# Kernel optimization log

Measured on AMD Instinct MI355X. Metric: run time of the kernel, lower is better.

The kernel has to match this reference:

```python
import jax, jax.numpy as jnp
import numpy as np

NUM_Q_HEADS = 32
NUM_KV_HEADS = 8
GROUP = NUM_Q_HEADS // NUM_KV_HEADS  # 4, matches hardcoded repeat_interleave(repeats=4)
HEAD_DIM = 128
ROPE_BASE = 10000.0


def _rope_cos_sin(seq_len, head_dim, dtype):
    # [S, D/2] angle tables for rotate-half RoPE
    inv_freq = 1.0 / (ROPE_BASE ** (jnp.arange(0, head_dim, 2, dtype=jnp.float32) / head_dim))
    ang = jnp.arange(seq_len, dtype=jnp.float32)[:, None] * inv_freq[None, :]
    return jnp.cos(ang).astype(dtype), jnp.sin(ang).astype(dtype)


def _apply_rope(x, cos, sin):
    # x: [B, S, H, D]; cos/sin: [S, D/2] broadcast over batch & heads
    x1, x2 = jnp.split(x, 2, axis=-1)
    c = cos[None, :, None, :]
    s = sin[None, :, None, :]
    return jnp.concatenate([x1 * c - x2 * s, x2 * c + x1 * s], axis=-1)


def setup_inputs() -> dict:
    key = jax.random.key(0)
    k1, k2, k3 = jax.random.split(key, 3)
    B, S, E = 2, 2048, 4096
    x = jax.random.normal(k1, (B, S, E), dtype=jnp.float32)
    w_in = jax.random.normal(k2, (6144, E), dtype=jnp.float32) * 0.02   # torch Linear weight [out, in]
    w_out = jax.random.normal(k3, (E, E), dtype=jnp.float32) * 0.02
    return {"x": x, "w_in": w_in, "w_out": w_out}


def reference(x, w_in, w_out):
    B, S, E = x.shape
    D = HEAD_DIM
    qkv = jnp.einsum('bse,fe->bsf', x, w_in)  # [B, S, 6144]
    parts = jnp.split(qkv, GROUP + 2, axis=-1)  # 6 equal chunks of width E//GROUP
    q = jnp.concatenate(parts[:GROUP], axis=-1).reshape(B, S, NUM_Q_HEADS, D)
    k = parts[GROUP].reshape(B, S, NUM_KV_HEADS, D)
    v = parts[GROUP + 1].reshape(B, S, NUM_KV_HEADS, D)

    cos, sin = _rope_cos_sin(S, D, x.dtype)
    q = _apply_rope(q, cos, sin)
    k = _apply_rope(k, cos, sin)

    # GQA without materializing repeated K/V: group q heads by kv head.
    # repeat_interleave(k, 4, dim=2) maps q head h -> kv head h // 4, i.e. q view [B,S,HKV,G,D]
    qg = q.reshape(B, S, NUM_KV_HEADS, GROUP, D)
    scale = 1.0 / jnp.sqrt(jnp.asarray(D, dtype=x.dtype))
    scores = jnp.einsum('bqhgd,bkhd->bhgqk', qg, k) * scale  # [B, HKV, G, S, S]
    causal = jnp.tril(jnp.ones((S, S), dtype=bool))
    scores = jnp.where(causal[None, None, None, :, :], scores, jnp.asarray(-1e30, dtype=scores.dtype))
    probs = jax.nn.softmax(scores, axis=-1)
    out = jnp.einsum('bhgqk,bkhd->bqhgd', probs, v)  # [B, S, HKV, G, D]
    out = out.reshape(B, S, E)
    return jnp.einsum('bse,fe->bsf', out, w_out)
```

## Files before the change

kernel.cpp:

```cpp
#include <hip/hip_runtime.h>
#include <hip/hip_bf16.h>
#include <stdint.h>

typedef unsigned short u16;
typedef __bf16 bf16x8 __attribute__((ext_vector_type(8)));
typedef u16 u16x8 __attribute__((ext_vector_type(8)));
typedef float f32x4 __attribute__((ext_vector_type(4)));

#define DEV __device__ __forceinline__
#define SBAR() asm volatile("s_barrier" ::: "memory")

DEV u16 f2bf(float f) {
  uint32_t u = __builtin_bit_cast(uint32_t, f);
  return (u16)((u + 0x7FFFu + ((u >> 16) & 1u)) >> 16);
}
DEV float bf2f(u16 h) { return __builtin_bit_cast(float, (uint32_t)h << 16); }

DEV void gload_lds16(const void* g, void* l) {
  __builtin_amdgcn_global_load_lds((const __attribute__((address_space(1))) uint32_t*)g,
                                   (__attribute__((address_space(3))) uint32_t*)l, 16, 0, 0);
}

__global__ void cvt_bf16(const float* __restrict__ in, u16* __restrict__ out, int n) {
  int i = (blockIdx.x * 256 + threadIdx.x) * 8;
  if (i >= n) return;
  const float4* p = reinterpret_cast<const float4*>(in + i);
  float4 a = p[0], b = p[1];
  u16x8 o;
  o[0] = f2bf(a.x); o[1] = f2bf(a.y); o[2] = f2bf(a.z); o[3] = f2bf(a.w);
  o[4] = f2bf(b.x); o[5] = f2bf(b.y); o[6] = f2bf(b.z); o[7] = f2bf(b.w);
  *reinterpret_cast<u16x8*>(out + i) = o;
}

__global__ void rope_table(float* __restrict__ ct, float* __restrict__ st) {
  int i = blockIdx.x * 256 + threadIdx.x;
  int s = i >> 6, d = i & 63;
  float invf = powf(10000.0f, -(float)d * (1.0f / 64.0f));
  float ang = (float)s * invf;
  ct[i] = cosf(ang);
  st[i] = sinf(ang);
}

__global__ void rope_apply(u16* __restrict__ qkv, const float* __restrict__ ct, const float* __restrict__ st) {
  int idx = blockIdx.x * 256 + threadIdx.x;
  int grp = idx & 7;
  int head = (idx >> 3) % 40;
  int row = idx / 320;
  int s = row & 2047;
  size_t f0 = head < 32 ? (size_t)head * 128 : (size_t)4096 + (size_t)(head - 32) * 128;
  u16* p = qkv + (size_t)row * 6144 + f0 + grp * 8;
  u16x8 a = *reinterpret_cast<const u16x8*>(p);
  u16x8 b = *reinterpret_cast<const u16x8*>(p + 64);
  const float4* cp = reinterpret_cast<const float4*>(ct + s * 64 + grp * 8);
  const float4* sp = reinterpret_cast<const float4*>(st + s * 64 + grp * 8);
  float4 c0 = cp[0], c1 = cp[1], s0 = sp[0], s1 = sp[1];
  float cc[8] = {c0.x, c0.y, c0.z, c0.w, c1.x, c1.y, c1.z, c1.w};
  float ss[8] = {s0.x, s0.y, s0.z, s0.w, s1.x, s1.y, s1.z, s1.w};
  u16x8 o1, o2;
#pragma unroll
  for (int i = 0; i < 8; i++) {
    float x1 = bf2f(a[i]), x2 = bf2f(b[i]);
    o1[i] = f2bf(x1 * cc[i] - x2 * ss[i]);
    o2[i] = f2bf(x2 * cc[i] + x1 * ss[i]);
  }
  *reinterpret_cast<u16x8*>(p) = o1;
  *reinterpret_cast<u16x8*>(p + 64) = o2;
}

__global__ void prep_vt(const u16* __restrict__ qkv, u16* __restrict__ vtg) {
  int id = blockIdx.x;
  int j = id & 31, kvh = (id >> 5) & 7, b = id >> 8;
  const int tid = threadIdx.x;
  const size_t rowB = (size_t)b * 2048;
  u16* img = vtg + (size_t)id * 8192;
#pragma unroll
  for (int p = 0; p < 4; p++) {
    int lin = p * 256 + tid;
    int d = lin >> 3, c = lin & 7;
    const u16* src = qkv + (rowB + j * 64 + c * 8) * 6144 + 5120 + kvh * 128 + d;
    u16x8 v;
#pragma unroll
    for (int i = 0; i < 8; i++) v[i] = src[(size_t)i * 6144];
    *reinterpret_cast<u16x8*>(img + d * 64 + ((c ^ (d & 7)) << 3)) = v;
  }
}

DEV void store_c(float* C, size_t idx, float v) { C[idx] = v; }
DEV void store_c(u16* C, size_t idx, float v) { C[idx] = f2bf(v); }

template <typename OutT>
__global__ __launch_bounds__(512, 2) void gemm256(const u16* __restrict__ A, const u16* __restrict__ B,
                                                  OutT* __restrict__ C, int M, int N, int K, int ldc) {
  __shared__ __align__(16) u16 lds[65536];
  char* LB = (char*)lds;
  const int tid = threadIdx.x;
  const int w = tid >> 6, lane = tid & 63;
  const int l15 = lane & 15, l4 = lane >> 4;
  const int wm = w >> 2, wn = w & 3;

  int nwg = gridDim.x;
  int q = nwg >> 3, rr = nwg & 7;
  int xcd = blockIdx.x & 7, idx = blockIdx.x >> 3;
  int sw = (xcd < rr ? xcd * (q + 1) : rr * (q + 1) + (xcd - rr) * q) + idx;
  int gxn = N >> 8;
  int by = sw / gxn, bx = sw - by * gxn;
  const int row0 = by << 8, col0 = bx << 8;
  const int NT = K >> 6;

  const int srow = w * 8 + (lane >> 3);
  const int sc16 = (lane & 7) ^ ((lane >> 3) & 7);
  const u16* gA = A + (size_t)(row0 + srow) * K + sc16 * 8;
  const u16* gB = B + (size_t)(col0 + srow) * K + sc16 * 8;

  const int fl = (l15 & 7) << 4;
  const int aoff = (wm * 128 + l15) * 128 + l4 * 16;
  const int boff = (wn * 64 + l15) * 128 + l4 * 16;

  f32x4 acc[8][4] = {};
  bf16x8 fA[4][2], fB0[2][2], fBc[2][2];

#define STAGE_A(kt, h, base)                                                      \
  {                                                                               \
    const u16* g_ = gA + (size_t)((h)*128) * K + (size_t)(kt)*64;                 \
    gload_lds16(g_, (base) + (h)*16384 + w * 1024);                               \
    gload_lds16(g_ + (size_t)64 * K, (base) + (h)*16384 + 8192 + w * 1024);       \
  }
#define STAGE_B(kt, h, base)                                                      \
  {                                                                               \
    const u16* g_ = gB + (size_t)((h)*128) * K + (size_t)(kt)*64;                 \
    gload_lds16(g_, (base) + (h)*16384 + w * 1024);                               \
    gload_lds16(g_ + (size_t)64 * K, (base) + (h)*16384 + 8192 + w * 1024);       \
  }
#define MFMA_Q(FB, MH, NH)                                                        \
  _Pragma("unroll") for (int kk = 0; kk < 2; kk++) {                              \
    _Pragma("unroll") for (int mf = 0; mf < 4; mf++) {                            \
      _Pragma("unroll") for (int nf = 0; nf < 2; nf++) {                          \
        acc[(MH)*4 + mf][(NH)*2 + nf] = __builtin_amdgcn_mfma_f32_16x16x32_bf16(  \
            fA[mf][kk], FB[nf][kk], acc[(MH)*4 + mf][(NH)*2 + nf], 0, 0, 0);      \
      }                                                                           \
    }                                                                             \
  }

  STAGE_A(0, 0, LB);
  STAGE_A(0, 1, LB);
  STAGE_B(0, 0, LB + 65536);
  STAGE_B(0, 1, LB + 65536);
  STAGE_A(1, 0, LB + 32768);
  STAGE_B(1, 0, LB + 98304);
  STAGE_B(1, 1, LB + 98304);
  asm volatile("s_waitcnt vmcnt(6)" ::: "memory");
  SBAR();

  for (int t = 0; t < NT; ++t) {
    char* ac = LB + (t & 1) * 32768;
    char* bc = LB + 65536 + (t & 1) * 32768;
    char* an = LB + ((t + 1) & 1) * 32768;

#pragma unroll
    for (int mf = 0; mf < 4; mf++)
#pragma unroll
      for (int kk = 0; kk < 2; kk++)
        fA[mf][kk] = *(const bf16x8*)(ac + ((aoff + mf * 2048 + kk * 64) ^ fl));
#pragma unroll
    for (int nf = 0; nf < 2; nf++)
#pragma unroll
      for (int kk = 0; kk < 2; kk++)
        fB0[nf][kk] = *(const bf16x8*)(bc + ((boff + nf * 2048 + kk * 64) ^ fl));
    if (t + 1 < NT) STAGE_A(t + 1, 1, an);
    asm volatile("s_waitcnt lgkmcnt(8)" ::: "memory");
    SBAR();
    asm volatile("s_waitcnt lgkmcnt(0)" ::: "memory");
    __builtin_amdgcn_sched_barrier(0);
    __builtin_amdgcn_s_setprio(1);
    MFMA_Q(fB0, 0, 0);
    __builtin_amdgcn_s_setprio(0);
    SBAR();

#pragma unroll
    for (int nf = 0; nf < 2; nf++)
#pragma unroll
      for (int kk = 0; kk < 2; kk++)
        fBc[nf][kk] = *(const bf16x8*)(bc + ((boff + (nf + 2) * 2048 + kk * 64) ^ fl));
    SBAR();
    asm volatile("s_waitcnt lgkmcnt(0)" ::: "memory");
    __builtin_amdgcn_sched_barrier(0);
    __builtin_amdgcn_s_setprio(1);
    MFMA_Q(fBc, 0, 1);
    __builtin_amdgcn_s_setprio(0);
    SBAR();

#pragma unroll
    for (int mf = 0; mf < 4; mf++)
#pragma unroll
      for (int kk = 0; kk < 2; kk++)
        fA[mf][kk] = *(const bf16x8*)(ac + ((aoff + (mf + 4) * 2048 + kk * 64) ^ fl));
    if (t + 2 < NT) STAGE_B(t + 2, 0, bc);
    SBAR();
    asm volatile("s_waitcnt lgkmcnt(0)" ::: "memory");
    __builtin_amdgcn_sched_barrier(0);
    __builtin_amdgcn_s_setprio(1);
    MFMA_Q(fBc, 1, 1);
    __builtin_amdgcn_s_setprio(0);
    SBAR();

    if (t + 2 < NT) {
      STAGE_A(t + 2, 0, ac);
      STAGE_B(t + 2, 1, bc);
    }
    SBAR();
    __builtin_amdgcn_s_setprio(1);
    MFMA_Q(fB0, 1, 0);
    __builtin_amdgcn_s_setprio(0);
    if (t <= NT - 3) {
      asm volatile("s_waitcnt vmcnt(6)" ::: "memory");
      SBAR();
    } else if (t < NT - 1) {
      asm volatile("s_waitcnt vmcnt(0)" ::: "memory");
      SBAR();
    }
  }

#pragma unroll
  for (int mf = 0; mf < 8; mf++)
#pragma unroll
    for (int nf = 0; nf < 4; nf++)
#pragma unroll
      for (int r = 0; r < 4; r++) {
        size_t row = (size_t)row0 + wm * 128 + mf * 16 + l4 * 4 + r;
        size_t col = (size_t)col0 + wn * 64 + nf * 16 + l15;
        store_c(C, row * (size_t)ldc + col, acc[mf][nf][r]);
      }
#undef STAGE_A
#undef STAGE_B
#undef MFMA_Q
}

__global__ __launch_bounds__(512, 2) void gemm_bn128(const u16* __restrict__ A, const u16* __restrict__ B,
                                                     u16* __restrict__ C, int M, int N, int K, int ldc) {
  __shared__ __align__(16) u16 lds[49152];
  char* LB = (char*)lds;
  const int tid = threadIdx.x;
  const int w = tid >> 6, lane = tid & 63;
  const int l15 = lane & 15, l4 = lane >> 4;
  const int wm = w >> 2, wn = w & 3;

  int nwg = gridDim.x;
  int q = nwg >> 3, rr = nwg & 7;
  int xcd = blockIdx.x & 7, idx = blockIdx.x >> 3;
  int sw = (xcd < rr ? xcd * (q + 1) : rr * (q + 1) + (xcd - rr) * q) + idx;
  int gxn = N >> 7;
  int by = sw / gxn, bx = sw - by * gxn;
  const int row0 = by << 8, col0 = bx << 7;
  const int NT = K >> 6;

  const int srow = w * 8 + (lane >> 3);
  const int sc16 = (lane & 7) ^ ((lane >> 3) & 7);
  const u16* gA = A + (size_t)(row0 + srow) * K + sc16 * 8;
  const u16* gB = B + (size_t)(col0 + srow) * K + sc16 * 8;

  const int fl = (l15 & 7) << 4;
  const int aoff = (wm * 128 + l15) * 128 + l4 * 16;
  const int boff = (wn * 32 + l15) * 128 + l4 * 16;

  f32x4 acc[8][2] = {};
  bf16x8 fA[4][2], fB[2][2];

#define STAGE_A(kt, h, base)                                                      \
  {                                                                               \
    const u16* g_ = gA + (size_t)((h)*128) * K + (size_t)(kt)*64;                 \
    gload_lds16(g_, (base) + (h)*16384 + w * 1024);                               \
    gload_lds16(g_ + (size_t)64 * K, (base) + (h)*16384 + 8192 + w * 1024);       \
  }
#define STAGE_B(kt, base)                                                         \
  {                                                                               \
    const u16* g_ = gB + (size_t)(kt)*64;                                         \
    gload_lds16(g_, (base) + w * 1024);                                           \
    gload_lds16(g_ + (size_t)64 * K, (base) + 8192 + w * 1024);                   \
  }

  STAGE_A(0, 0, LB);
  STAGE_A(0, 1, LB);
  STAGE_B(0, LB + 65536);
  STAGE_A(1, 0, LB + 32768);
  STAGE_B(1, LB + 65536 + 16384);
  asm volatile("s_waitcnt vmcnt(4)" ::: "memory");
  SBAR();

  for (int t = 0; t < NT; ++t) {
    char* ac = LB + (t & 1) * 32768;
    char* bc = LB + 65536 + (t & 1) * 16384;
    char* an = LB + ((t + 1) & 1) * 32768;

#pragma unroll
    for (int mf = 0; mf < 4; mf++)
#pragma unroll
      for (int kk = 0; kk < 2; kk++)
        fA[mf][kk] = *(const bf16x8*)(ac + ((aoff + mf * 2048 + kk * 64) ^ fl));
#pragma unroll
    for (int nf = 0; nf < 2; nf++)
#pragma unroll
      for (int kk = 0; kk < 2; kk++)
        fB[nf][kk] = *(const bf16x8*)(bc + ((boff + nf * 2048 + kk * 64) ^ fl));
    if (t + 1 < NT) STAGE_A(t + 1, 1, an);
    asm volatile("s_waitcnt lgkmcnt(8)" ::: "memory");
    SBAR();
    asm volatile("s_waitcnt lgkmcnt(0)" ::: "memory");
    __builtin_amdgcn_sched_barrier(0);
    __builtin_amdgcn_s_setprio(1);
#pragma unroll
    for (int kk = 0; kk < 2; kk++)
#pragma unroll
      for (int mf = 0; mf < 4; mf++)
#pragma unroll
        for (int nf = 0; nf < 2; nf++)
          acc[mf][nf] = __builtin_amdgcn_mfma_f32_16x16x32_bf16(fA[mf][kk], fB[nf][kk], acc[mf][nf], 0, 0, 0);
    __builtin_amdgcn_s_setprio(0);
    SBAR();

#pragma unroll
    for (int mf = 0; mf < 4; mf++)
#pragma unroll
      for (int kk = 0; kk < 2; kk++)
        fA[mf][kk] = *(const bf16x8*)(ac + ((aoff + (mf + 4) * 2048 + kk * 64) ^ fl));
    if (t + 2 < NT) {
      STAGE_A(t + 2, 0, ac);
      STAGE_B(t + 2, bc);
    }
    SBAR();
    asm volatile("s_waitcnt lgkmcnt(0)" ::: "memory");
    __builtin_amdgcn_sched_barrier(0);
    __builtin_amdgcn_s_setprio(1);
#pragma unroll
    for (int kk = 0; kk < 2; kk++)
#pragma unroll
      for (int mf = 0; mf < 4; mf++)
#pragma unroll
        for (int nf = 0; nf < 2; nf++)
          acc[mf + 4][nf] = __builtin_amdgcn_mfma_f32_16x16x32_bf16(fA[mf][kk], fB[nf][kk], acc[mf + 4][nf], 0, 0, 0);
    __builtin_amdgcn_s_setprio(0);
    if (t <= NT - 3) {
      asm volatile("s_waitcnt vmcnt(4)" ::: "memory");
      SBAR();
    } else if (t < NT - 1) {
      asm volatile("s_waitcnt vmcnt(0)" ::: "memory");
      SBAR();
    }
  }

#pragma unroll
  for (int mf = 0; mf < 8; mf++)
#pragma unroll
    for (int nf = 0; nf < 2; nf++)
#pragma unroll
      for (int r = 0; r < 4; r++) {
        size_t row = (size_t)row0 + wm * 128 + mf * 16 + l4 * 4 + r;
        size_t col = (size_t)col0 + wn * 32 + nf * 16 + l15;
        C[row * (size_t)ldc + col] = f2bf(acc[mf][nf][r]);
      }
#undef STAGE_A
#undef STAGE_B
}

__global__ __launch_bounds__(256, 2) void attn_fwd(const u16* __restrict__ qkv,
                                                   const u16* __restrict__ vtg,
                                                   u16* __restrict__ out) {
  constexpr int S = 2048, F = 6144, E = 4096;
  __shared__ __align__(16) u16 Kt[2 * 8192];
  __shared__ __align__(16) u16 Vt[2 * 8192];
  __shared__ __align__(16) u16 Pl[4 * 2048];

  const int tid = threadIdx.x;
  const int w = tid >> 6, lane = tid & 63;
  const int l15 = lane & 15, l4 = lane >> 4;
  const int pair = blockIdx.x;
  const int b = blockIdx.y >> 5, h = blockIdx.y & 31, kvh = h >> 2;
  const size_t rowB = (size_t)b * S;
  const float sc = 0.08838834764831845f * 1.4426950408889634f;
  const int sgn = tid >> 4, sgc = tid & 15;
  char* PlW = ((char*)Pl) + w * 4096;
  const size_t vtb = (size_t)(b * 8 + kvh) * 32 * 8192;

  auto stage = [&](int j, int buf) {
    char* kd = ((char*)Kt) + buf * 16384 + w * 1024;
    char* vd = ((char*)Vt) + buf * 16384 + w * 1024;
    const u16* vs = vtg + vtb + (size_t)j * 8192 + tid * 8;
#pragma unroll
    for (int p = 0; p < 4; p++) {
      int n = p * 16 + sgn;
      const u16* g = qkv + (rowB + j * 64 + n) * F + 4096 + kvh * 128 + (sgc ^ (n & 7)) * 8;
      gload_lds16(g, kd + p * 4096);
      gload_lds16(vs + p * 2048, vd + p * 4096);
    }
  };

  for (int half = 0; half < 2; ++half) {
    const int t = half ? 15 - pair : pair;
    const int nt = 2 * t + 2;
    const int r0 = t * 128;

    bf16x8 qf[2][4];
    {
      const u16* qp = qkv + (rowB + r0 + w * 32 + l15) * F + h * 128 + l4 * 8;
#pragma unroll
      for (int m = 0; m < 2; m++)
#pragma unroll
        for (int kk = 0; kk < 4; kk++)
          qf[m][kk] = *reinterpret_cast<const bf16x8*>(qp + (size_t)m * 16 * F + kk * 32);
    }

    f32x4 acco[2][8] = {};
    float m_r[2][4], l_r[2][4];
#pragma unroll
    for (int m = 0; m < 2; m++)
#pragma unroll
      for (int r = 0; r < 4; r++) { m_r[m][r] = -1e30f; l_r[m][r] = 0.f; }

    stage(0, 0);
    __syncthreads();

    for (int j = 0; j < nt; ++j) {
      const int cur = j & 1;
      if (j + 1 < nt) stage(j + 1, cur ^ 1);

      const char* kbase = ((const char*)Kt) + cur * 16384;
      f32x4 accs[2][4] = {};
      __builtin_amdgcn_s_setprio(1);
#pragma unroll
      for (int ns = 0; ns < 4; ns++) {
        int n = ns * 16 + l15;
        const char* kb = kbase + n * 256;
#pragma unroll
        for (int kk = 0; kk < 4; kk++) {
          bf16x8 kf = *reinterpret_cast<const bf16x8*>(kb + (((kk * 4 + l4) ^ (n & 7)) << 4));
          accs[0][ns] = __builtin_amdgcn_mfma_f32_16x16x32_bf16(qf[0][kk], kf, accs[0][ns], 0, 0, 0);
          accs[1][ns] = __builtin_amdgcn_mfma_f32_16x16x32_bf16(qf[1][kk], kf, accs[1][ns], 0, 0, 0);
        }
      }
      __builtin_amdgcn_s_setprio(0);

      const int qb = r0 + w * 32 + l4 * 4;
      const int kvb = j * 64 + l15;
      if (j >= 2 * t) {
#pragma unroll
        for (int m = 0; m < 2; m++)
#pragma unroll
          for (int ns = 0; ns < 4; ns++)
#pragma unroll
            for (int r = 0; r < 4; r++)
              accs[m][ns][r] = (kvb + ns * 16 > qb + m * 16 + r) ? -1e30f : accs[m][ns][r] * sc;
      } else {
#pragma unroll
        for (int m = 0; m < 2; m++)
#pragma unroll
          for (int ns = 0; ns < 4; ns++)
#pragma unroll
            for (int r = 0; r < 4; r++) accs[m][ns][r] *= sc;
      }

      float tm[2][4];
#pragma unroll
      for (int m = 0; m < 2; m++)
#pragma unroll
        for (int r = 0; r < 4; r++) {
          float a = fmaxf(fmaxf(accs[m][0][r], accs[m][1][r]), fmaxf(accs[m][2][r], accs[m][3][r]));
          a = fmaxf(a, __shfl_xor(a, 1));
          a = fmaxf(a, __shfl_xor(a, 2));
          a = fmaxf(a, __shfl_xor(a, 4));
          a = fmaxf(a, __shfl_xor(a, 8));
          tm[m][r] = a;
        }
      int needb = 0;
#pragma unroll
      for (int m = 0; m < 2; m++)
#pragma unroll
        for (int r = 0; r < 4; r++) needb |= (tm[m][r] > m_r[m][r] + 8.0f) ? 1 : 0;
      if (__any(needb)) {
#pragma unroll
        for (int m = 0; m < 2; m++)
#pragma unroll
          for (int r = 0; r < 4; r++) {
            float m2 = fmaxf(m_r[m][r], tm[m][r]);
            float fr = exp2f(m_r[m][r] - m2);
            m_r[m][r] = m2;
            l_r[m][r] *= fr;
#pragma unroll
            for (int ns = 0; ns < 8; ns++) acco[m][ns][r] *= fr;
          }
      }
      float ps[2][4] = {};
#pragma unroll
      for (int m = 0; m < 2; m++)
#pragma unroll
        for (int ns = 0; ns < 4; ns++)
#pragma unroll
          for (int r = 0; r < 4; r++) {
            float p = exp2f(accs[m][ns][r] - m_r[m][r]);
            ps[m][r] += p;
            int row = m * 16 + l4 * 4 + r;
            int kv2 = (ns * 16 + l15) * 2;
            *(u16*)(PlW + row * 128 + (kv2 ^ ((row & 7) << 4))) = f2bf(p);
          }
#pragma unroll
      for (int m = 0; m < 2; m++)
#pragma unroll
        for (int r = 0; r < 4; r++) {
          float s2 = ps[m][r];
          s2 += __shfl_xor(s2, 1);
          s2 += __shfl_xor(s2, 2);
          s2 += __shfl_xor(s2, 4);
          s2 += __shfl_xor(s2, 8);
          l_r[m][r] += s2;
        }

      const char* vbase = ((const char*)Vt) + cur * 16384;
      bf16x8 pf[2][2];
#pragma unroll
      for (int m = 0; m < 2; m++)
#pragma unroll
        for (int kk = 0; kk < 2; kk++) {
          int row = m * 16 + l15;
          pf[m][kk] = *reinterpret_cast<const bf16x8*>(PlW + row * 128 + (((kk * 4 + l4) ^ (row & 7)) << 4));
        }
      __builtin_amdgcn_s_setprio(1);
#pragma unroll
      for (int ns = 0; ns < 8; ns++) {
        int d = ns * 16 + l15;
        const char* vb = vbase + d * 128;
#pragma unroll
        for (int kk = 0; kk < 2; kk++) {
          bf16x8 vf = *reinterpret_cast<const bf16x8*>(vb + (((kk * 4 + l4) ^ (d & 7)) << 4));
          acco[0][ns] = __builtin_amdgcn_mfma_f32_16x16x32_bf16(pf[0][kk], vf, acco[0][ns], 0, 0, 0);
          acco[1][ns] = __builtin_amdgcn_mfma_f32_16x16x32_bf16(pf[1][kk], vf, acco[1][ns], 0, 0, 0);
        }
      }
      __builtin_amdgcn_s_setprio(0);

      __syncthreads();
    }

#pragma unroll
    for (int m = 0; m < 2; m++)
#pragma unroll
      for (int r = 0; r < 4; r++) {
        float inv = 1.f / l_r[m][r];
        size_t row = rowB + r0 + w * 32 + m * 16 + l4 * 4 + r;
#pragma unroll
        for (int ns = 0; ns < 8; ns++)
          out[row * E + h * 128 + ns * 16 + l15] = f2bf(acco[m][ns][r] * inv);
      }
  }
}

extern "C" void kernel_launch(void* const* d_in, const int* in_sizes, int n_in,
                              void* d_out, int out_size, void* d_ws, size_t ws_size,
                              hipStream_t stream) {
  const float* x = (const float*)d_in[0];
  const float* w_in = (const float*)d_in[1];
  const float* w_out = (const float*)d_in[2];
  float* out = (float*)d_out;
  char* ws = (char*)d_ws;

  u16* xb = (u16*)(ws);
  u16* wib = (u16*)(ws + 33554432ull);
  u16* wob = (u16*)(ws + 83886080ull);
  u16* qkvb = (u16*)(ws + 117440512ull);
  float* ct = (float*)(ws + 167772160ull);
  float* st = ct + 2048 * 64;
  u16* attnb = xb;
  u16* vtg = wib;

  cvt_bf16<<<8192, 256, 0, stream>>>(x, xb, 16777216);
  cvt_bf16<<<12288, 256, 0, stream>>>(w_in, wib, 25165824);
  cvt_bf16<<<8192, 256, 0, stream>>>(w_out, wob, 16777216);
  rope_table<<<512, 256, 0, stream>>>(ct, st);
  gemm256<u16><<<256, 512, 0, stream>>>(xb, wib, qkvb, 4096, 4096, 4096, 6144);
  gemm_bn128<<<256, 512, 0, stream>>>(xb, wib + (size_t)4096 * 4096, qkvb + 4096, 4096, 2048, 4096, 6144);
  rope_apply<<<5120, 256, 0, stream>>>(qkvb, ct, st);
  prep_vt<<<512, 256, 0, stream>>>(qkvb, vtg);
  attn_fwd<<<dim3(8, 64), 256, 0, stream>>>(qkvb, vtg, attnb);
  gemm256<float><<<256, 512, 0, stream>>>(attnb, wob, out, 4096, 4096, 4096, 4096);
}
```

Baseline: 570.7 us.

## Use transposed 32x32 MFMA scores to keep P in registers, drop LDS round-trip

The attention kernel moves from 16x16x32 to 32x32x16 bf16 MFMAs and computes S^T = K·Q^T, so each lane owns one query column. Row max and row sum then reduce mostly within a lane plus one cross-half shuffle. P is packed to bf16 with v_cvt_pk_bf16_f32 and rearranged with v_permlane32_swap into the A-operand layout for the PV MFMA, which removes the per-wave P scratch buffer in LDS and its stores and loads. In exchange, the rescale and final normalisation need ds_bpermute broadcasts per accumulator row, and the 32x32 accumulators may raise register pressure.

```diff
diff --git a/kernel.cpp b/kernel.cpp
--- a/kernel.cpp
+++ b/kernel.cpp
@@ -6,6 +6,8 @@
 typedef __bf16 bf16x8 __attribute__((ext_vector_type(8)));
 typedef u16 u16x8 __attribute__((ext_vector_type(8)));
 typedef float f32x4 __attribute__((ext_vector_type(4)));
+typedef float f32x16 __attribute__((ext_vector_type(16)));
+typedef uint32_t u32x4 __attribute__((ext_vector_type(4)));
 
 #define DEV __device__ __forceinline__
 #define SBAR() asm volatile("s_barrier" ::: "memory")
@@ -19,6 +21,15 @@
 DEV void gload_lds16(const void* g, void* l) {
   __builtin_amdgcn_global_load_lds((const __attribute__((address_space(1))) uint32_t*)g,
                                    (__attribute__((address_space(3))) uint32_t*)l, 16, 0, 0);
+}
+
+DEV uint32_t cvtpk(float lo, float hi) {
+  uint32_t r;
+  asm("v_cvt_pk_bf16_f32 %0, %1, %2" : "=v"(r) : "v"(lo), "v"(hi));
+  return r;
+}
+DEV void plswap(uint32_t& a, uint32_t& b) {
+  asm("v_permlane32_swap_b32 %0, %1" : "+v"(a), "+v"(b));
 }
 
 __global__ void cvt_bf16(const float* __restrict__ in, u16* __restrict__ out, int n) {
@@ -367,17 +378,15 @@
   constexpr int S = 2048, F = 6144, E = 4096;
   __shared__ __align__(16) u16 Kt[2 * 8192];
   __shared__ __align__(16) u16 Vt[2 * 8192];
-  __shared__ __align__(16) u16 Pl[4 * 2048];
 
   const int tid = threadIdx.x;
   const int w = tid >> 6, lane = tid & 63;
-  const int l15 = lane & 15, l4 = lane >> 4;
+  const int l31 = lane & 31, hi = lane >> 5;
   const int pair = blockIdx.x;
   const int b = blockIdx.y >> 5, h = blockIdx.y & 31, kvh = h >> 2;
   const size_t rowB = (size_t)b * S;
   const float sc = 0.08838834764831845f * 1.4426950408889634f;
   const int sgn = tid >> 4, sgc = tid & 15;
-  char* PlW = ((char*)Pl) + w * 4096;
   const size_t vtb = (size_t)(b * 8 + kvh) * 32 * 8192;
 
   auto stage = [&](int j, int buf) {
@@ -397,23 +406,17 @@
     const int t = half ? 15 - pair : pair;
     const int nt = 2 * t + 2;
     const int r0 = t * 128;
-
-    bf16x8 qf[2][4];
+    const int qg = r0 + w * 32 + l31;
+
+    bf16x8 qf[8];
     {
-      const u16* qp = qkv + (rowB + r0 + w * 32 + l15) * F + h * 128 + l4 * 8;
-#pragma unroll
-      for (int m = 0; m < 2; m++)
-#pragma unroll
-        for (int kk = 0; kk < 4; kk++)
-          qf[m][kk] = *reinterpret_cast<const bf16x8*>(qp + (size_t)m * 16 * F + kk * 32);
-    }
-
-    f32x4 acco[2][8] = {};
-    float m_r[2][4], l_r[2][4];
-#pragma unroll
-    for (int m = 0; m < 2; m++)
-#pragma unroll
-      for (int r = 0; r < 4; r++) { m_r[m][r] = -1e30f; l_r[m][r] = 0.f; }
+      const u16* qp = qkv + (rowB + qg) * F + h * 128 + hi * 8;
+#pragma unroll
+      for (int ds = 0; ds < 8; ds++) qf[ds] = *reinterpret_cast<const bf16x8*>(qp + ds * 16);
+    }
+
+    f32x16 acco[4] = {};
+    float m = -1e30f, l = 0.f;
 
     stage(0, 0);
     __syncthreads();
@@ -423,131 +426,115 @@
       if (j + 1 < nt) stage(j + 1, cur ^ 1);
 
       const char* kbase = ((const char*)Kt) + cur * 16384;
-      f32x4 accs[2][4] = {};
+      f32x16 s0 = {}, s1 = {};
       __builtin_amdgcn_s_setprio(1);
 #pragma unroll
-      for (int ns = 0; ns < 4; ns++) {
-        int n = ns * 16 + l15;
-        const char* kb = kbase + n * 256;
-#pragma unroll
-        for (int kk = 0; kk < 4; kk++) {
-          bf16x8 kf = *reinterpret_cast<const bf16x8*>(kb + (((kk * 4 + l4) ^ (n & 7)) << 4));
-          accs[0][ns] = __builtin_amdgcn_mfma_f32_16x16x32_bf16(qf[0][kk], kf, accs[0][ns], 0, 0, 0);
-          accs[1][ns] = __builtin_amdgcn_mfma_f32_16x16x32_bf16(qf[1][kk], kf, accs[1][ns], 0, 0, 0);
+      for (int ds = 0; ds < 8; ds++) {
+        int ch = ((2 * ds + hi) ^ (l31 & 7)) << 4;
+        bf16x8 k0 = *reinterpret_cast<const bf16x8*>(kbase + l31 * 256 + ch);
+        bf16x8 k1 = *reinterpret_cast<const bf16x8*>(kbase + (32 + l31) * 256 + ch);
+        s0 = __builtin_amdgcn_mfma_f32_32x32x16_bf16(k0, qf[ds], s0, 0, 0, 0);
+        s1 = __builtin_amdgcn_mfma_f32_32x32x16_bf16(k1, qf[ds], s1, 0, 0, 0);
+      }
+      __builtin_amdgcn_s_setprio(0);
+
+      f32x16 px0, px1;
+      if (j >= 2 * t) {
+#pragma unroll
+        for (int rg = 0; rg < 16; rg++) {
+          int kv0 = j * 64 + (rg & 3) + 8 * (rg >> 2) + 4 * hi;
+          px0[rg] = (kv0 > qg) ? -1e30f : s0[rg] * sc;
+          px1[rg] = (kv0 + 32 > qg) ? -1e30f : s1[rg] * sc;
+        }
+      } else {
+#pragma unroll
+        for (int rg = 0; rg < 16; rg++) {
+          px0[rg] = s0[rg] * sc;
+          px1[rg] = s1[rg] * sc;
         }
       }
-      __builtin_amdgcn_s_setprio(0);
-
-      const int qb = r0 + w * 32 + l4 * 4;
-      const int kvb = j * 64 + l15;
-      if (j >= 2 * t) {
-#pragma unroll
-        for (int m = 0; m < 2; m++)
-#pragma unroll
-          for (int ns = 0; ns < 4; ns++)
-#pragma unroll
-            for (int r = 0; r < 4; r++)
-              accs[m][ns][r] = (kvb + ns * 16 > qb + m * 16 + r) ? -1e30f : accs[m][ns][r] * sc;
-      } else {
-#pragma unroll
-        for (int m = 0; m < 2; m++)
-#pragma unroll
-          for (int ns = 0; ns < 4; ns++)
-#pragma unroll
-            for (int r = 0; r < 4; r++) accs[m][ns][r] *= sc;
-      }
-
-      float tm[2][4];
-#pragma unroll
-      for (int m = 0; m < 2; m++)
-#pragma unroll
-        for (int r = 0; r < 4; r++) {
-          float a = fmaxf(fmaxf(accs[m][0][r], accs[m][1][r]), fmaxf(accs[m][2][r], accs[m][3][r]));
-          a = fmaxf(a, __shfl_xor(a, 1));
-          a = fmaxf(a, __shfl_xor(a, 2));
-          a = fmaxf(a, __shfl_xor(a, 4));
-          a = fmaxf(a, __shfl_xor(a, 8));
-          tm[m][r] = a;
-        }
-      int needb = 0;
-#pragma unroll
-      for (int m = 0; m < 2; m++)
-#pragma unroll
-        for (int r = 0; r < 4; r++) needb |= (tm[m][r] > m_r[m][r] + 8.0f) ? 1 : 0;
-      if (__any(needb)) {
-#pragma unroll
-        for (int m = 0; m < 2; m++)
-#pragma unroll
-          for (int r = 0; r < 4; r++) {
-            float m2 = fmaxf(m_r[m][r], tm[m][r]);
-            float fr = exp2f(m_r[m][r] - m2);
-            m_r[m][r] = m2;
-            l_r[m][r] *= fr;
-#pragma unroll
-            for (int ns = 0; ns < 8; ns++) acco[m][ns][r] *= fr;
-          }
-      }
-      float ps[2][4] = {};
-#pragma unroll
-      for (int m = 0; m < 2; m++)
-#pragma unroll
-        for (int ns = 0; ns < 4; ns++)
-#pragma unroll
-          for (int r = 0; r < 4; r++) {
-            float p = exp2f(accs[m][ns][r] - m_r[m][r]);
-            ps[m][r] += p;
-            int row = m * 16 + l4 * 4 + r;
-            int kv2 = (ns * 16 + l15) * 2;
-            *(u16*)(PlW + row * 128 + (kv2 ^ ((row & 7) << 4))) = f2bf(p);
-          }
-#pragma unroll
-      for (int m = 0; m < 2; m++)
-#pragma unroll
-        for (int r = 0; r < 4; r++) {
-          float s2 = ps[m][r];
-          s2 += __shfl_xor(s2, 1);
-          s2 += __shfl_xor(s2, 2);
-          s2 += __shfl_xor(s2, 4);
-          s2 += __shfl_xor(s2, 8);
-          l_r[m][r] += s2;
-        }
-
-      const char* vbase = ((const char*)Vt) + cur * 16384;
-      bf16x8 pf[2][2];
-#pragma unroll
-      for (int m = 0; m < 2; m++)
-#pragma unroll
-        for (int kk = 0; kk < 2; kk++) {
-          int row = m * 16 + l15;
-          pf[m][kk] = *reinterpret_cast<const bf16x8*>(PlW + row * 128 + (((kk * 4 + l4) ^ (row & 7)) << 4));
-        }
-      __builtin_amdgcn_s_setprio(1);
-#pragma unroll
-      for (int ns = 0; ns < 8; ns++) {
-        int d = ns * 16 + l15;
-        const char* vb = vbase + d * 128;
-#pragma unroll
-        for (int kk = 0; kk < 2; kk++) {
-          bf16x8 vf = *reinterpret_cast<const bf16x8*>(vb + (((kk * 4 + l4) ^ (d & 7)) << 4));
-          acco[0][ns] = __builtin_amdgcn_mfma_f32_16x16x32_bf16(pf[0][kk], vf, acco[0][ns], 0, 0, 0);
-          acco[1][ns] = __builtin_amdgcn_mfma_f32_16x16x32_bf16(pf[1][kk], vf, acco[1][ns], 0, 0, 0);
+
+      float mt[8];
+#pragma unroll
+      for (int i = 0; i < 8; i++)
+        mt[i] = fmaxf(fmaxf(px0[i], px0[i + 8]), fmaxf(px1[i], px1[i + 8]));
+#pragma unroll
+      for (int stp = 4; stp; stp >>= 1)
+#pragma unroll
+        for (int i = 0; i < stp; i++) mt[i] = fmaxf(mt[i], mt[i + stp]);
+      float pm = fmaxf(mt[0], __shfl_xor(mt[0], 32));
+
+      if (__any(pm > m + 8.0f)) {
+        float mn = fmaxf(m, pm);
+        float fr = exp2f(m - mn);
+        m = mn;
+        l *= fr;
+#pragma unroll
+        for (int rg = 0; rg < 16; rg++) {
+          int qrow = (rg & 3) + 8 * (rg >> 2) + 4 * hi;
+          float frq = __builtin_bit_cast(
+              float, __builtin_amdgcn_ds_bpermute(qrow << 2, __builtin_bit_cast(int, fr)));
+          acco[0][rg] *= frq;
+          acco[1][rg] *= frq;
+          acco[2][rg] *= frq;
+          acco[3][rg] *= frq;
         }
       }
+
+#pragma unroll
+      for (int rg = 0; rg < 16; rg++) {
+        px0[rg] = exp2f(px0[rg] - m);
+        px1[rg] = exp2f(px1[rg] - m);
+      }
+      float at[8];
+#pragma unroll
+      for (int i = 0; i < 8; i++)
+        at[i] = (px0[i] + px0[i + 8]) + (px1[i] + px1[i + 8]);
+#pragma unroll
+      for (int stp = 4; stp; stp >>= 1)
+#pragma unroll
+        for (int i = 0; i < stp; i++) at[i] += at[i + stp];
+      l += at[0] + __shfl_xor(at[0], 32);
+
+      const char* vbase = ((const char*)Vt) + cur * 16384;
+      __builtin_amdgcn_s_setprio(1);
+#define PV_STEP(PH, SS)                                                               \
+  {                                                                                   \
+    uint32_t X0 = cvtpk(PH[((SS)&1) * 8 + 0], PH[((SS)&1) * 8 + 1]);                  \
+    uint32_t Y0 = cvtpk(PH[((SS)&1) * 8 + 4], PH[((SS)&1) * 8 + 5]);                  \
+    uint32_t X1 = cvtpk(PH[((SS)&1) * 8 + 2], PH[((SS)&1) * 8 + 3]);                  \
+    uint32_t Y1 = cvtpk(PH[((SS)&1) * 8 + 6], PH[((SS)&1) * 8 + 7]);                  \
+    plswap(X0, Y0);                                                                   \
+    plswap(X1, Y1);                                                                   \
+    u32x4 pw = {X0, X1, Y0, Y1};                                                      \
+    bf16x8 pa = __builtin_bit_cast(bf16x8, pw);                                       \
+    _Pragma("unroll") for (int df = 0; df < 4; df++) {                                \
+      bf16x8 vf = *reinterpret_cast<const bf16x8*>(                                   \
+          vbase + (32 * df + l31) * 128 + (((2 * (SS) + hi) ^ (l31 & 7)) << 4));      \
+      acco[df] = __builtin_amdgcn_mfma_f32_32x32x16_bf16(pa, vf, acco[df], 0, 0, 0);  \
+    }                                                                                 \
+  }
+      PV_STEP(px0, 0)
+      PV_STEP(px0, 1)
+      PV_STEP(px1, 2)
+      PV_STEP(px1, 3)
+#undef PV_STEP
       __builtin_amdgcn_s_setprio(0);
 
       __syncthreads();
     }
 
-#pragma unroll
-    for (int m = 0; m < 2; m++)
-#pragma unroll
-      for (int r = 0; r < 4; r++) {
-        float inv = 1.f / l_r[m][r];
-        size_t row = rowB + r0 + w * 32 + m * 16 + l4 * 4 + r;
-#pragma unroll
-        for (int ns = 0; ns < 8; ns++)
-          out[row * E + h * 128 + ns * 16 + l15] = f2bf(acco[m][ns][r] * inv);
-      }
+    float linv = 1.f / l;
+#pragma unroll
+    for (int rg = 0; rg < 16; rg++) {
+      int qrow = (rg & 3) + 8 * (rg >> 2) + 4 * hi;
+      float lv = __builtin_bit_cast(
+          float, __builtin_amdgcn_ds_bpermute(qrow << 2, __builtin_bit_cast(int, linv)));
+      size_t row = rowB + r0 + w * 32 + qrow;
+      u16* op = out + row * E + h * 128 + l31;
+#pragma unroll
+      for (int df = 0; df < 4; df++) op[df * 32] = f2bf(acco[df][rg] * lv);
+    }
   }
 }
 
```

After: 511.1 us. 10.4% less time.
